# Kernel tuning notes

Hardware: AMD Instinct MI355X
Metric: run time of the kernel (lower is better)

Reference implementation:

```python
import jax, jax.numpy as jnp
import numpy as np

B, M, D, H, K, V = 4, 2048, 1024, 16, 64, 64

def setup_inputs() -> dict:
    key = jax.random.key(0)
    ks = jax.random.split(key, 5)
    return {
        "x": jax.random.normal(ks[0], (B, M, D), dtype=jnp.float32),
        "P_q": jax.random.normal(ks[1], (H, D, K), dtype=jnp.float32) * 0.02,
        "P_k": jax.random.normal(ks[2], (H, D, K), dtype=jnp.float32) * 0.02,
        "P_v": jax.random.normal(ks[3], (H, D, V), dtype=jnp.float32) * 0.02,
        "P_o": jax.random.normal(ks[4], (H, D, V), dtype=jnp.float32) * 0.02,
    }

def reference(x, P_q, P_k, P_v, P_o):
    # QKV projections: [b,m,d] x [h,d,k] -> [b,h,m,k]
    Q = jnp.einsum('bmd,hdk->bhmk', x, P_q)
    Kt = jnp.einsum('bmd,hdk->bhmk', x, P_k)
    Vt = jnp.einsum('bmd,hdv->bhmv', x, P_v)
    scale = 1.0 / jnp.sqrt(jnp.asarray(K, dtype=x.dtype))
    logits = jnp.einsum('bhmk,bhnk->bhmn', Q, Kt) * scale  # [b,h,m,m]
    m = logits.shape[-1]
    causal = jnp.tril(jnp.ones((m, m), dtype=bool))  # allow j <= i
    logits = jnp.where(causal[None, None], logits, jnp.asarray(-jnp.inf, dtype=logits.dtype))
    weights = jax.nn.softmax(logits, axis=-1)
    o = jnp.einsum('bhmn,bhnv->bhmv', weights, Vt)
    y = jnp.einsum('bhmv,hdv->bmd', o, P_o)
    return y
```

## Files before the change

kernel.cpp:

```cpp
#include <hip/hip_runtime.h>
#include <hip/hip_bf16.h>

#define B_  4
#define M_  2048
#define D_  1024
#define H_  16

typedef __attribute__((ext_vector_type(8)))  short bf16x8;
typedef __attribute__((ext_vector_type(4)))  float f32x4;
typedef __attribute__((ext_vector_type(16))) float f32x16;
typedef __attribute__((ext_vector_type(4)))  unsigned short u16x4;
typedef __attribute__((ext_vector_type(2)))  unsigned int uint2v;

#define MFMA16(a, b, c) __builtin_amdgcn_mfma_f32_16x16x32_bf16((a), (b), (c), 0, 0, 0)
#define MFMA32(a, b, c) __builtin_amdgcn_mfma_f32_32x32x16_bf16((a), (b), (c), 0, 0, 0)

#define QSCALE 0.18033688011112042f

__device__ __forceinline__ unsigned short f2b(float f) {
  union { float f; unsigned u; } v; v.f = f;
  unsigned r = v.u + 0x7FFF + ((v.u >> 16) & 1);
  return (unsigned short)(r >> 16);
}

__device__ __forceinline__ unsigned cvtpk(float lo, float hi) {
  unsigned r;
  asm("v_cvt_pk_bf16_f32 %0, %1, %2" : "=v"(r) : "v"(lo), "v"(hi));
  return r;
}

__device__ __forceinline__ int swzb(int byte) {
  return byte ^ (((byte >> 7) & 7) << 4);
}

#define SWZ256(L) ((L) ^ ((((L) >> 8) & 15) << 4))

#define GLOAD16(gsrc, ldst)                                                     \
  __builtin_amdgcn_global_load_lds(                                             \
      (const __attribute__((address_space(1))) void*)(gsrc),                    \
      (__attribute__((address_space(3))) void*)(ldst), 16, 0, 0)

__global__ __launch_bounds__(256) void convert_x_kernel(
    const float* __restrict__ x, short* __restrict__ xb) {
  const size_t i = ((size_t)blockIdx.x * 256 + threadIdx.x) * 8;
  float4 a = *(const float4*)(x + i);
  float4 b = *(const float4*)(x + i + 4);
  bf16x8 o;
  o[0] = (short)f2b(a.x); o[1] = (short)f2b(a.y); o[2] = (short)f2b(a.z); o[3] = (short)f2b(a.w);
  o[4] = (short)f2b(b.x); o[5] = (short)f2b(b.y); o[6] = (short)f2b(b.z); o[7] = (short)f2b(b.w);
  *(bf16x8*)(xb + i) = o;
}

__global__ __launch_bounds__(256) void convert_w_kernel(
    const float* __restrict__ Pq, const float* __restrict__ Pk,
    const float* __restrict__ Pv, short* __restrict__ Wt) {
  const int idx = blockIdx.x * 256 + threadIdx.x;
  const int n = idx >> 8, d0 = (idx & 255) * 4;
  const int which = n >> 10, h = (n >> 6) & 15, kc = n & 63;
  const float* P = (which == 0) ? Pq : (which == 1) ? Pk : Pv;
  const float* p = P + ((size_t)h * D_ + d0) * 64 + kc;
  u16x4 o;
  o[0] = f2b(p[0]); o[1] = f2b(p[64]); o[2] = f2b(p[128]); o[3] = f2b(p[192]);
  *(u16x4*)(Wt + (size_t)n * D_ + d0) = o;
}

__global__ __launch_bounds__(256) void convert_wo_kernel(
    const float* __restrict__ Po, short* __restrict__ Wo) {
  const int idx = blockIdx.x * 256 + threadIdx.x;
  const int d = idx >> 8, hv0 = (idx & 255) * 4;
  const int h = hv0 >> 6, v = hv0 & 63;
  float4 a = *(const float4*)(Po + ((size_t)h * D_ + d) * 64 + v);
  u16x4 o;
  o[0] = f2b(a.x); o[1] = f2b(a.y); o[2] = f2b(a.z); o[3] = f2b(a.w);
  *(u16x4*)(Wo + (size_t)d * 1024 + hv0) = o;
}

__device__ __forceinline__ void gemm_body_128x128(
    const char* __restrict__ Agc, const char* __restrict__ Bgc,
    short* AsBase, short* BsBase, int t, int w, int lane,
    f32x4 (&acc)[4][4])
{
  const int wr = (w >> 1) * 64, wc = (w & 1) * 64;
  const int lrow = lane & 15, lgrp = lane >> 4;

  auto stage = [&](int bi, int kt) {
    const int d2 = kt * 128;
#pragma unroll
    for (int i = 0; i < 4; ++i) {
      const int L = i * 4096 + t * 16;
      const int row = L >> 7;
      const int cs = (L & 127) ^ ((row & 7) << 4);
      GLOAD16(Agc + (size_t)row * 2048 + d2 + cs, (char*)AsBase + bi * 16384 + L);
      GLOAD16(Bgc + (size_t)row * 2048 + d2 + cs, (char*)BsBase + bi * 16384 + L);
    }
  };

  stage(0, 0);

  for (int kt = 0; kt < 16; ++kt) {
    const int cur = kt & 1;
    __builtin_amdgcn_s_barrier();
    if (kt + 1 < 16) {
      stage(cur ^ 1, kt + 1);
      asm volatile("s_waitcnt vmcnt(8)" ::: "memory");
    } else {
      asm volatile("s_waitcnt vmcnt(0)" ::: "memory");
    }
    __builtin_amdgcn_s_barrier();

    const char* Ac = (const char*)AsBase + cur * 16384;
    const char* Bc = (const char*)BsBase + cur * 16384;
#pragma unroll
    for (int ks = 0; ks < 2; ++ks) {
      bf16x8 a[4], b[4];
      const int cb = ks * 64 + lgrp * 16;
#pragma unroll
      for (int f = 0; f < 4; ++f) {
        a[f] = *(const bf16x8*)(Ac + swzb((wr + f * 16 + lrow) * 128 + cb));
        b[f] = *(const bf16x8*)(Bc + swzb((wc + f * 16 + lrow) * 128 + cb));
      }
      __builtin_amdgcn_s_setprio(1);
#pragma unroll
      for (int mf = 0; mf < 4; ++mf)
#pragma unroll
        for (int nf = 0; nf < 4; ++nf)
          acc[mf][nf] = MFMA16(a[mf], b[nf], acc[mf][nf]);
      __builtin_amdgcn_s_setprio(0);
    }
  }
}

__global__ __launch_bounds__(256) void qkv_gemm_kernel(
    const short* __restrict__ xb, const short* __restrict__ Wt,
    short* __restrict__ Qw, short* __restrict__ Kw, short* __restrict__ Vt) {
  __shared__ short As[2][8192];
  __shared__ short Bs[2][8192];
  const int bid = blockIdx.x;
  const int xcd = bid & 7, slot = bid >> 3;
  const int m0 = (xcd * 8 + (slot & 7)) * 128;
  const int n0 = (slot >> 3) * 128;
  const int t = threadIdx.x, lane = t & 63, w = t >> 6;

  f32x4 acc[4][4] = {};
  gemm_body_128x128((const char*)xb + (size_t)m0 * 2048,
                    (const char*)Wt + (size_t)n0 * 2048,
                    &As[0][0], &Bs[0][0], t, w, lane, acc);

  const int wr = (w >> 1) * 64, wc = (w & 1) * 64;
  const int lrow = lane & 15, lgrp = lane >> 4;
#pragma unroll
  for (int nf = 0; nf < 4; ++nf) {
    const int n = n0 + wc + nf * 16 + lrow;
    const int which = n >> 10, h = (n >> 6) & 15, kc = n & 63;
#pragma unroll
    for (int mf = 0; mf < 4; ++mf) {
      const int row0 = m0 + wr + mf * 16 + lgrp * 4;
      const int b = row0 >> 11, mm = row0 & 2047;
      const int bh = b * 16 + h;
      if (which == 2) {
        u16x4 o;
        o[0] = f2b(acc[mf][nf][0]); o[1] = f2b(acc[mf][nf][1]);
        o[2] = f2b(acc[mf][nf][2]); o[3] = f2b(acc[mf][nf][3]);
        *(u16x4*)(Vt + ((size_t)bh * 64 + kc) * M_ + mm) = o;
      } else {
        short* outp = (which == 0 ? Qw : Kw) + ((size_t)bh * M_ + mm) * 64 + kc;
        const float scale = (which == 0) ? QSCALE : 1.0f;
#pragma unroll
        for (int r = 0; r < 4; ++r)
          outp[(size_t)r * 64] = (short)f2b(acc[mf][nf][r] * scale);
      }
    }
  }
}

__global__ __launch_bounds__(256) void out_gemm_kernel(
    const short* __restrict__ O2, const short* __restrict__ Wo,
    float* __restrict__ y) {
  __shared__ short As[2][8192];
  __shared__ short Bs[2][8192];
  const int bid = blockIdx.x;
  const int xcd = bid & 7, slot = bid >> 3;
  const int m0 = (xcd * 8 + (slot & 7)) * 128;
  const int n0 = (slot >> 3) * 128;
  const int t = threadIdx.x, lane = t & 63, w = t >> 6;

  f32x4 acc[4][4] = {};
  gemm_body_128x128((const char*)O2 + (size_t)m0 * 2048,
                    (const char*)Wo + (size_t)n0 * 2048,
                    &As[0][0], &Bs[0][0], t, w, lane, acc);

  const int wr = (w >> 1) * 64, wc = (w & 1) * 64;
  const int lrow = lane & 15, lgrp = lane >> 4;
#pragma unroll
  for (int mf = 0; mf < 4; ++mf)
#pragma unroll
    for (int nf = 0; nf < 4; ++nf) {
      const int n = n0 + wc + nf * 16 + lrow;
      const int row0 = m0 + wr + mf * 16 + lgrp * 4;
#pragma unroll
      for (int r = 0; r < 4; ++r)
        y[(size_t)(row0 + r) * 1024 + n] = acc[mf][nf][r];
    }
}

__device__ __forceinline__ void softmax_chunk(
    f32x16& s0, f32x16& s1, f32x16& o0, f32x16& o1,
    float& mrun, float& lrun, bf16x8 (&pf)[4])
{
  float tm[16];
#pragma unroll
  for (int r = 0; r < 16; ++r) tm[r] = fmaxf(s0[r], s1[r]);
#pragma unroll
  for (int st = 8; st > 0; st >>= 1)
#pragma unroll
    for (int r = 0; r < 8; ++r)
      if (r < st) tm[r] = fmaxf(tm[r], tm[r + st]);
  uint2v pm = __builtin_amdgcn_permlane32_swap(
      __float_as_uint(tm[0]), __float_as_uint(tm[0]), false, false);
  const float mtile = fmaxf(__uint_as_float(pm[0]), __uint_as_float(pm[1]));

  if (!__all(mtile <= mrun + 8.0f)) {
    const float mnew = fmaxf(mrun, mtile);
    const float alpha = __builtin_amdgcn_exp2f(mrun - mnew);
    mrun = mnew;
    lrun *= alpha;
    o0 *= alpha;
    o1 *= alpha;
  }
#pragma unroll
  for (int r = 0; r < 16; ++r) {
    s0[r] = __builtin_amdgcn_exp2f(s0[r] - mrun);
    s1[r] = __builtin_amdgcn_exp2f(s1[r] - mrun);
  }
#pragma unroll
  for (int c = 0; c < 4; ++c) {
    const f32x16& sv = (c < 2) ? s0 : s1;
    const int rb = (c & 1) * 8;
    unsigned a0 = cvtpk(sv[rb + 0], sv[rb + 1]);
    unsigned a1 = cvtpk(sv[rb + 2], sv[rb + 3]);
    unsigned b0 = cvtpk(sv[rb + 4], sv[rb + 5]);
    unsigned b1 = cvtpk(sv[rb + 6], sv[rb + 7]);
    uint2v t0 = __builtin_amdgcn_permlane32_swap(a0, b0, false, false);
    uint2v t1 = __builtin_amdgcn_permlane32_swap(a1, b1, false, false);
    union { unsigned u[4]; bf16x8 v; } pk;
    pk.u[0] = t0[0]; pk.u[1] = t1[0]; pk.u[2] = t0[1]; pk.u[3] = t1[1];
    pf[c] = pk.v;
  }
}

__global__ __launch_bounds__(256) void attn_kernel(
    const short* __restrict__ Qw, const short* __restrict__ Kw,
    const short* __restrict__ Vt, short* __restrict__ O2) {
  __shared__ short Ks[2][64 * 64];
  __shared__ short Vs[2][64 * 64];

  const int bid = blockIdx.x;
  const int chunk = 15 - (bid >> 6);
  const int bh = bid & 63;
  const int q0 = chunk * 128;

  const int t = threadIdx.x, lane = t & 63, w = t >> 6;
  const int l31 = lane & 31, hi = lane >> 5;
  const int qw0 = q0 + w * 32;
  const int qabs = qw0 + l31;

  bf16x8 qfrag[4];
#pragma unroll
  for (int kc = 0; kc < 4; ++kc)
    qfrag[kc] = *(const bf16x8*)(Qw + ((size_t)bh * M_ + qabs) * 64 + kc * 16 + hi * 8);

  f32x16 o0 = {}, o1 = {};
  float mrun = -3.0e38f, lrun = 0.f;

  const char* Kg = (const char*)Kw + (size_t)bh * M_ * 128;
  const char* Vg = (const char*)Vt + (size_t)bh * 64 * M_ * 2;

  auto stage = [&](int bi, int j0_) {
#pragma unroll
    for (int i = 0; i < 2; ++i) {
      const int L  = i * 4096 + t * 16;
      const int Ls = SWZ256(L);
      const int row = Ls >> 7, col = Ls & 127;
      GLOAD16(Kg + (size_t)(j0_ + row) * 128 + col, (char*)Ks[bi] + i * 4096 + w * 1024);
      GLOAD16(Vg + (size_t)row * (M_ * 2) + (size_t)j0_ * 2 + col, (char*)Vs[bi] + i * 4096 + w * 1024);
    }
  };

  const int nt = (q0 + 128) >> 6;
  stage(0, 0);

  bf16x8 ones;
#pragma unroll
  for (int e = 0; e < 8; ++e) ones[e] = (short)0x3F80;

  for (int tt = 0; tt < nt; ++tt) {
    const int j0 = tt << 6;
    const int cur = tt & 1;
    __builtin_amdgcn_s_barrier();
    if (tt + 1 < nt) {
      stage(cur ^ 1, j0 + 64);
      asm volatile("s_waitcnt vmcnt(4)" ::: "memory");
    } else {
      asm volatile("s_waitcnt vmcnt(0)" ::: "memory");
    }
    __builtin_amdgcn_s_barrier();
    if (j0 >= qw0 + 32) continue;

    const char* Kc = (const char*)Ks[cur];
    const char* Vc = (const char*)Vs[cur];

    f32x16 s0 = {}, s1 = {};
    __builtin_amdgcn_s_setprio(1);
#pragma unroll
    for (int kc = 0; kc < 4; ++kc) {
      bf16x8 kf0 = *(const bf16x8*)(Kc + SWZ256(l31 * 128 + kc * 32 + hi * 16));
      s0 = MFMA32(kf0, qfrag[kc], s0);
      bf16x8 kf1 = *(const bf16x8*)(Kc + SWZ256((32 + l31) * 128 + kc * 32 + hi * 16));
      s1 = MFMA32(kf1, qfrag[kc], s1);
    }
    __builtin_amdgcn_s_setprio(0);

    if (j0 + 64 > qw0) {
#pragma unroll
      for (int r = 0; r < 16; ++r) {
        const int k0 = j0 + (r & 3) + 8 * (r >> 2) + 4 * hi;
        if (k0 > qabs)      s0[r] = -3.0e38f;
        if (k0 + 32 > qabs) s1[r] = -3.0e38f;
      }
    }

    bf16x8 pf[4];
    softmax_chunk(s0, s1, o0, o1, mrun, lrun, pf);

    f32x16 lacc = {};
    __builtin_amdgcn_s_setprio(1);
#pragma unroll
    for (int c = 0; c < 4; ++c) {
      bf16x8 vf0 = *(const bf16x8*)(Vc + SWZ256(l31 * 128 + c * 32 + hi * 16));
      o0 = MFMA32(vf0, pf[c], o0);
      bf16x8 vf1 = *(const bf16x8*)(Vc + SWZ256((32 + l31) * 128 + c * 32 + hi * 16));
      o1 = MFMA32(vf1, pf[c], o1);
      lacc = MFMA32(ones, pf[c], lacc);
    }
    __builtin_amdgcn_s_setprio(0);
    lrun += lacc[0];
  }

  const int b = bh >> 4, h = bh & 15;
  const float inv = 1.0f / lrun;
  short* orow = O2 + ((size_t)b * M_ + qabs) * 1024 + h * 64;
#pragma unroll
  for (int vb = 0; vb < 2; ++vb) {
    const f32x16& o = vb ? o1 : o0;
#pragma unroll
    for (int g = 0; g < 4; ++g) {
      const int vbase = vb * 32 + 8 * g + 4 * hi;
      u16x4 pkt;
      pkt[0] = f2b(o[g * 4 + 0] * inv);
      pkt[1] = f2b(o[g * 4 + 1] * inv);
      pkt[2] = f2b(o[g * 4 + 2] * inv);
      pkt[3] = f2b(o[g * 4 + 3] * inv);
      *(u16x4*)(orow + vbase) = pkt;
    }
  }
}

extern "C" void kernel_launch(void* const* d_in, const int* in_sizes, int n_in,
                              void* d_out, int out_size, void* d_ws, size_t ws_size,
                              hipStream_t stream) {
  const float* x  = (const float*)d_in[0];
  const float* Pq = (const float*)d_in[1];
  const float* Pk = (const float*)d_in[2];
  const float* Pv = (const float*)d_in[3];
  const float* Po = (const float*)d_in[4];
  float* y = (float*)d_out;

  short* ws = (short*)d_ws;
  const size_t NX = (size_t)B_ * M_ * D_;
  short* xb  = ws;                 ws += NX;
  short* Wt  = ws;                 ws += (size_t)3072 * 1024;
  short* Wo  = ws;                 ws += (size_t)1024 * 1024;
  short* Qw  = ws;                 ws += NX;
  short* Kw  = ws;                 ws += NX;
  short* Vt  = ws;                 ws += NX;
  short* O2  = ws;                 ws += NX;

  convert_x_kernel <<<4096, 256, 0, stream>>>(x, xb);
  convert_w_kernel <<<3072, 256, 0, stream>>>(Pq, Pk, Pv, Wt);
  convert_wo_kernel<<<1024, 256, 0, stream>>>(Po, Wo);
  qkv_gemm_kernel  <<<1536, 256, 0, stream>>>(xb, Wt, Qw, Kw, Vt);
  attn_kernel      <<<1024, 256, 0, stream>>>(Qw, Kw, Vt, O2);
  out_gemm_kernel  <<<512,  256, 0, stream>>>(O2, Wo, y);
}
```

Baseline: 183.6 us.

## Enlarge QKV GEMM to 256x256 tiles with 8 waves and deeper staging

Rewrites the QKV projection GEMM to use 256x256 output tiles computed by 512-thread blocks (8 waves, each owning a 128x64 sub-tile). A 128KB LDS buffer holds two k-steps split into 64-wide halves, and global loads for upcoming halves are interleaved across the eight compute phases. The aim is more arithmetic per byte staged and better overlap of loads with MFMA work. The cost is much higher LDS and register use per block, which limits the kernel to one block per CU. The grid of 384 blocks also leaves an uneven final wave.

After: 217.7 us. +18.6%, slower.

```diff
diff --git a/kernel.cpp b/kernel.cpp
--- a/kernel.cpp
+++ b/kernel.cpp
@@ -75,86 +75,100 @@
   *(u16x4*)(Wo + (size_t)d * 1024 + hv0) = o;
 }
 
-__device__ __forceinline__ void gemm_body_128x128(
-    const char* __restrict__ Agc, const char* __restrict__ Bgc,
-    short* AsBase, short* BsBase, int t, int w, int lane,
-    f32x4 (&acc)[4][4])
-{
-  const int wr = (w >> 1) * 64, wc = (w & 1) * 64;
-  const int lrow = lane & 15, lgrp = lane >> 4;
-
-  auto stage = [&](int bi, int kt) {
-    const int d2 = kt * 128;
-#pragma unroll
-    for (int i = 0; i < 4; ++i) {
-      const int L = i * 4096 + t * 16;
-      const int row = L >> 7;
-      const int cs = (L & 127) ^ ((row & 7) << 4);
-      GLOAD16(Agc + (size_t)row * 2048 + d2 + cs, (char*)AsBase + bi * 16384 + L);
-      GLOAD16(Bgc + (size_t)row * 2048 + d2 + cs, (char*)BsBase + bi * 16384 + L);
-    }
-  };
-
-  stage(0, 0);
-
-  for (int kt = 0; kt < 16; ++kt) {
-    const int cur = kt & 1;
-    __builtin_amdgcn_s_barrier();
-    if (kt + 1 < 16) {
-      stage(cur ^ 1, kt + 1);
-      asm volatile("s_waitcnt vmcnt(8)" ::: "memory");
-    } else {
-      asm volatile("s_waitcnt vmcnt(0)" ::: "memory");
-    }
-    __builtin_amdgcn_s_barrier();
-
-    const char* Ac = (const char*)AsBase + cur * 16384;
-    const char* Bc = (const char*)BsBase + cur * 16384;
-#pragma unroll
-    for (int ks = 0; ks < 2; ++ks) {
-      bf16x8 a[4], b[4];
-      const int cb = ks * 64 + lgrp * 16;
-#pragma unroll
-      for (int f = 0; f < 4; ++f) {
-        a[f] = *(const bf16x8*)(Ac + swzb((wr + f * 16 + lrow) * 128 + cb));
-        b[f] = *(const bf16x8*)(Bc + swzb((wc + f * 16 + lrow) * 128 + cb));
-      }
-      __builtin_amdgcn_s_setprio(1);
-#pragma unroll
-      for (int mf = 0; mf < 4; ++mf)
-#pragma unroll
-        for (int nf = 0; nf < 4; ++nf)
-          acc[mf][nf] = MFMA16(a[mf], b[nf], acc[mf][nf]);
-      __builtin_amdgcn_s_setprio(0);
-    }
-  }
-}
-
-__global__ __launch_bounds__(256) void qkv_gemm_kernel(
+__global__ __launch_bounds__(512, 2) void qkv_gemm_kernel(
     const short* __restrict__ xb, const short* __restrict__ Wt,
     short* __restrict__ Qw, short* __restrict__ Kw, short* __restrict__ Vt) {
-  __shared__ short As[2][8192];
-  __shared__ short Bs[2][8192];
+  __shared__ __align__(16) char lds[131072];
   const int bid = blockIdx.x;
   const int xcd = bid & 7, slot = bid >> 3;
-  const int m0 = (xcd * 8 + (slot & 7)) * 128;
-  const int n0 = (slot >> 3) * 128;
+  const int m0 = (xcd * 4 + (slot & 3)) * 256;
+  const int n0 = (slot >> 2) * 256;
   const int t = threadIdx.x, lane = t & 63, w = t >> 6;
-
-  f32x4 acc[4][4] = {};
-  gemm_body_128x128((const char*)xb + (size_t)m0 * 2048,
-                    (const char*)Wt + (size_t)n0 * 2048,
-                    &As[0][0], &Bs[0][0], t, w, lane, acc);
-
-  const int wr = (w >> 1) * 64, wc = (w & 1) * 64;
+  const int wm = w >> 2, wn = w & 3;
   const int lrow = lane & 15, lgrp = lane >> 4;
+
+  const char* Agc = (const char*)xb + (size_t)m0 * 2048;
+  const char* Bgc = (const char*)Wt + (size_t)n0 * 2048;
+
+  auto stageA = [&](int b, int ks, int kt) {
+#pragma unroll
+    for (int i = 0; i < 2; ++i) {
+      const int L = i * 8192 + t * 16;
+      const int sk = L >> 12, row = (L & 4095) >> 4;
+      GLOAD16(Agc + (size_t)row * 2048 + kt * 128 + ks * 64 + sk * 16,
+              lds + (b * 2 + ks) * 16384 + i * 8192 + w * 1024);
+    }
+  };
+  auto stageB = [&](int b, int ks, int kt) {
+#pragma unroll
+    for (int i = 0; i < 2; ++i) {
+      const int L = i * 8192 + t * 16;
+      const int sk = L >> 12, row = (L & 4095) >> 4;
+      GLOAD16(Bgc + (size_t)row * 2048 + kt * 128 + ks * 64 + sk * 16,
+              lds + 65536 + (b * 2 + ks) * 16384 + i * 8192 + w * 1024);
+    }
+  };
+
+  f32x4 acc[8][4] = {};
+
+  stageA(0, 0, 0); stageB(0, 0, 0);
+  stageA(0, 1, 0); stageB(0, 1, 0);
+  stageA(1, 0, 1); stageB(1, 0, 1);
+  asm volatile("s_waitcnt vmcnt(8)" ::: "memory");
+  __builtin_amdgcn_s_barrier();
+
+  for (int it = 0; it < 8; ++it) {
+    const int k1 = 2 * it + 1;
+    const int k2 = (2 * it + 2 > 15) ? 15 : 2 * it + 2;
+    const int k3 = (2 * it + 3 > 15) ? 15 : 2 * it + 3;
+    bf16x8 bfr[4];
+#pragma unroll
+    for (int p = 0; p < 8; ++p) {
+      const int buf = p >> 2, ks = (p >> 1) & 1, mh = p & 1;
+      const char* Ar = lds + (buf * 2 + ks) * 16384;
+      const char* Br = lds + 65536 + (buf * 2 + ks) * 16384;
+      bf16x8 afr[4];
+#pragma unroll
+      for (int f = 0; f < 4; ++f)
+        afr[f] = *(const bf16x8*)(Ar + lgrp * 4096 +
+                                  (wm * 128 + (mh * 4 + f) * 16 + lrow) * 16);
+      if (mh == 0) {
+#pragma unroll
+        for (int f = 0; f < 4; ++f)
+          bfr[f] = *(const bf16x8*)(Br + lgrp * 4096 +
+                                    (wn * 64 + f * 16 + lrow) * 16);
+      }
+      if (p == 0) stageA(1, 1, k1);
+      if (p == 1) stageB(1, 1, k1);
+      if (p == 2) stageA(0, 0, k2);
+      if (p == 3) stageB(0, 0, k2);
+      if (p == 4) stageA(0, 1, k2);
+      if (p == 5) stageB(0, 1, k2);
+      if (p == 6) stageA(1, 0, k3);
+      if (p == 7) stageB(1, 0, k3);
+
+      __builtin_amdgcn_s_barrier();
+      __builtin_amdgcn_s_setprio(1);
+#pragma unroll
+      for (int f = 0; f < 4; ++f)
+#pragma unroll
+        for (int nf = 0; nf < 4; ++nf)
+          acc[mh * 4 + f][nf] = MFMA16(afr[f], bfr[nf], acc[mh * 4 + f][nf]);
+      __builtin_amdgcn_s_setprio(0);
+      if (mh == 1) asm volatile("s_waitcnt vmcnt(8)" ::: "memory");
+      __builtin_amdgcn_s_barrier();
+    }
+  }
+  asm volatile("s_waitcnt vmcnt(0)" ::: "memory");
+
+  const int which = n0 >> 10;
 #pragma unroll
   for (int nf = 0; nf < 4; ++nf) {
-    const int n = n0 + wc + nf * 16 + lrow;
-    const int which = n >> 10, h = (n >> 6) & 15, kc = n & 63;
-#pragma unroll
-    for (int mf = 0; mf < 4; ++mf) {
-      const int row0 = m0 + wr + mf * 16 + lgrp * 4;
+    const int n = n0 + wn * 64 + nf * 16 + lrow;
+    const int h = (n >> 6) & 15, kc = n & 63;
+#pragma unroll
+    for (int mf = 0; mf < 8; ++mf) {
+      const int row0 = m0 + wm * 128 + mf * 16 + lgrp * 4;
       const int b = row0 >> 11, mm = row0 & 2047;
       const int bh = b * 16 + h;
       if (which == 2) {
@@ -169,6 +183,61 @@
         for (int r = 0; r < 4; ++r)
           outp[(size_t)r * 64] = (short)f2b(acc[mf][nf][r] * scale);
       }
+    }
+  }
+}
+
+__device__ __forceinline__ void gemm_body_128x128(
+    const char* __restrict__ Agc, const char* __restrict__ Bgc,
+    short* AsBase, short* BsBase, int t, int w, int lane,
+    f32x4 (&acc)[4][4])
+{
+  const int wr = (w >> 1) * 64, wc = (w & 1) * 64;
+  const int lrow = lane & 15, lgrp = lane >> 4;
+
+  auto stage = [&](int bi, int kt) {
+    const int d2 = kt * 128;
+#pragma unroll
+    for (int i = 0; i < 4; ++i) {
+      const int L = i * 4096 + t * 16;
+      const int row = L >> 7;
+      const int cs = (L & 127) ^ ((row & 7) << 4);
+      GLOAD16(Agc + (size_t)row * 2048 + d2 + cs, (char*)AsBase + bi * 16384 + L);
+      GLOAD16(Bgc + (size_t)row * 2048 + d2 + cs, (char*)BsBase + bi * 16384 + L);
+    }
+  };
+
+  stage(0, 0);
+
+  for (int kt = 0; kt < 16; ++kt) {
+    const int cur = kt & 1;
+    __builtin_amdgcn_s_barrier();
+    if (kt + 1 < 16) {
+      stage(cur ^ 1, kt + 1);
+      asm volatile("s_waitcnt vmcnt(8)" ::: "memory");
+    } else {
+      asm volatile("s_waitcnt vmcnt(0)" ::: "memory");
+    }
+    __builtin_amdgcn_s_barrier();
+
+    const char* Ac = (const char*)AsBase + cur * 16384;
+    const char* Bc = (const char*)BsBase + cur * 16384;
+#pragma unroll
+    for (int ks = 0; ks < 2; ++ks) {
+      bf16x8 a[4], b[4];
+      const int cb = ks * 64 + lgrp * 16;
+#pragma unroll
+      for (int f = 0; f < 4; ++f) {
+        a[f] = *(const bf16x8*)(Ac + swzb((wr + f * 16 + lrow) * 128 + cb));
+        b[f] = *(const bf16x8*)(Bc + swzb((wc + f * 16 + lrow) * 128 + cb));
+      }
+      __builtin_amdgcn_s_setprio(1);
+#pragma unroll
+      for (int mf = 0; mf < 4; ++mf)
+#pragma unroll
+        for (int nf = 0; nf < 4; ++nf)
+          acc[mf][nf] = MFMA16(a[mf], b[nf], acc[mf][nf]);
+      __builtin_amdgcn_s_setprio(0);
     }
   }
 }
@@ -388,7 +457,7 @@
   convert_x_kernel <<<4096, 256, 0, stream>>>(x, xb);
   convert_w_kernel <<<3072, 256, 0, stream>>>(Pq, Pk, Pv, Wt);
   convert_wo_kernel<<<1024, 256, 0, stream>>>(Po, Wo);
-  qkv_gemm_kernel  <<<1536, 256, 0, stream>>>(xb, Wt, Qw, Kw, Vt);
+  qkv_gemm_kernel  <<<384,  512, 0, stream>>>(xb, Wt, Qw, Kw, Vt);
   attn_kernel      <<<1024, 256, 0, stream>>>(Qw, Kw, Vt, O2);
   out_gemm_kernel  <<<512,  256, 0, stream>>>(O2, Wo, y);
 }
```
